# Performance work log

Measured on AMD Instinct MI355X. Metric: run time of the kernel, lower is better.

Reference implementation:

```python
import jax, jax.numpy as jnp
import numpy as np

N, E, D, L = 50000, 800000, 256, 3  # nodes, edges, feature dim, layers


def setup_inputs() -> dict:
    key = jax.random.key(0)
    k = jax.random.split(key, 5)
    edge_index = jax.random.randint(k[0], (2, E), 0, N)  # row0=src, row1=tgt (PyG COO)
    x_init = jax.random.normal(k[1], (N, D), dtype=jnp.float32)
    s = 1.0 / np.sqrt(D).astype(np.float32)  # Glorot-ish init scale
    W_l = jax.random.uniform(k[2], (L, D, D), minval=-s, maxval=s, dtype=jnp.float32)
    W_r = jax.random.uniform(k[3], (L, D, D), minval=-s, maxval=s, dtype=jnp.float32)
    b = jnp.zeros((L, D), dtype=jnp.float32)
    return {"edge_index": edge_index, "x_init": x_init, "W_l": W_l, "W_r": W_r, "b": b}


def reference(edge_index, x_init, W_l, W_r, b):
    src, tgt = edge_index[0], edge_index[1]
    # mean-aggregation normalizer, computed once (degree of each target node)
    deg = jax.ops.segment_sum(jnp.ones((E,), jnp.float32), tgt, num_segments=N)
    inv_deg = jnp.where(deg > 0, 1.0 / deg, 0.0)[:, None]  # [N,1]

    def sage_conv(x, i):
        # PyG SAGEConv (aggr='mean'): out = lin_l(mean_j x_j) + lin_r(x_i)
        agg = jax.ops.segment_sum(x[src], tgt, num_segments=N) * inv_deg  # [N,D]
        return agg @ W_l[i] + x @ W_r[i] + b[i]

    x = x_init
    x_list = []
    for i in range(L - 1):
        x = jax.nn.relu(sage_conv(x, i) + x)  # residual then ReLU
        x_list.append(x)
        # dropout p=0.0 -> identity
    x = sage_conv(x, L - 1) + x  # final layer with residual, no ReLU
    x_list.append(x)
    return jnp.concatenate(x_list, axis=1)  # [N, L*D] concat of all layer outputs
```

## Files before the change

kernel.cpp:

```cpp
#include <hip/hip_runtime.h>
#include <hip/hip_bf16.h>
#include <stdint.h>

#define NN 50000
#define EE 800000
#define DD 256
#define LL 3
#define NBLK 49
#define NPAD 50176

using floatx4 = __attribute__((ext_vector_type(4))) float;
using shortx8 = __attribute__((ext_vector_type(8))) short;

union U8 { shortx8 v; uint32_t u[4]; };

typedef __attribute__((address_space(1))) const unsigned int gu32;
typedef __attribute__((address_space(3))) unsigned int lu32;
__device__ __forceinline__ void async_copy16(const void* g, void* l) {
    __builtin_amdgcn_global_load_lds((gu32*)g, (lu32*)l, 16, 0, 0);
}

__device__ __forceinline__ uint16_t f2bf(float f) {
    __hip_bfloat16 h = __float2bfloat16(f);
    return *reinterpret_cast<uint16_t*>(&h);
}
__device__ __forceinline__ float bf2f(uint32_t u) {
    union { uint32_t u32; float f; } cv; cv.u32 = (u & 0xffffu) << 16; return cv.f;
}

__global__ void k_count(const int* __restrict__ tgt, int* __restrict__ deg) {
    int e = blockIdx.x * 256 + threadIdx.x;
    if (e < EE) atomicAdd(&deg[tgt[e]], 1);
}

__global__ void k_scan1(const int* __restrict__ deg, int* __restrict__ row_start,
                        int* __restrict__ bsum) {
    __shared__ int wsum[16];
    int t = threadIdx.x, w = t >> 6, lane = t & 63;
    int i = blockIdx.x * 1024 + t;
    int v = (i < NN) ? deg[i] : 0;
    int s = v;
#pragma unroll
    for (int off = 1; off < 64; off <<= 1) {
        int u = __shfl_up(s, off);
        if (lane >= off) s += u;
    }
    if (lane == 63) wsum[w] = s;
    __syncthreads();
    if (t < 16) {
        int ws = wsum[t];
#pragma unroll
        for (int off = 1; off < 16; off <<= 1) {
            int u = __shfl_up(ws, off);
            if (t >= off) ws += u;
        }
        wsum[t] = ws;
    }
    __syncthreads();
    int off = (w > 0) ? wsum[w - 1] : 0;
    if (i < NN) row_start[i] = off + s - v;
    if (t == 1023) bsum[blockIdx.x] = off + s;
}

__global__ void k_scan2(int* __restrict__ bsum, int* __restrict__ row_start) {
    int t = threadIdx.x;
    int v = (t < NBLK) ? bsum[t] : 0;
    int s = v;
#pragma unroll
    for (int off = 1; off < 64; off <<= 1) {
        int u = __shfl_up(s, off);
        if (t >= off) s += u;
    }
    if (t < NBLK) bsum[t] = s - v;
    if (t == 0) row_start[NN] = EE;
}

__global__ void k_init2(const int* __restrict__ deg, const int* __restrict__ bsum,
                        int* __restrict__ row_start, int* __restrict__ cursor,
                        float* __restrict__ invd) {
    int i = blockIdx.x * 1024 + threadIdx.x;
    if (i < NN) {
        int r = row_start[i] + bsum[blockIdx.x];
        row_start[i] = r;
        cursor[i] = r;
        int d = deg[i];
        invd[i] = d > 0 ? 1.0f / (float)d : 0.0f;
    }
}

__global__ void k_scatter(const int* __restrict__ src, const int* __restrict__ tgt,
                          int* __restrict__ cursor, int* __restrict__ csr) {
    int e = blockIdx.x * 256 + threadIdx.x;
    if (e < EE) {
        int p = atomicAdd(&cursor[tgt[e]], 1);
        csr[p] = src[e];
    }
}

__global__ void k_wprep(const float* __restrict__ Wl, const float* __restrict__ Wr,
                        uint16_t* __restrict__ wtl_hi, uint16_t* __restrict__ wtl_lo,
                        uint16_t* __restrict__ wtr_hi, uint16_t* __restrict__ wtr_lo) {
    int d = blockIdx.x * 256 + threadIdx.x;
    int i = d >> 16, n = (d >> 8) & 255, k = d & 255;
    int s = (i << 16) | (k << 8) | n;
    float wl = Wl[s];
    float wr = Wr[s] + ((n == k) ? 1.0f : 0.0f);
    uint32_t ul = __float_as_uint(wl), ur = __float_as_uint(wr);
    wtl_hi[d] = (uint16_t)(ul >> 16);
    wtl_lo[d] = f2bf(wl - __uint_as_float(ul & 0xFFFF0000u));
    wtr_hi[d] = (uint16_t)(ur >> 16);
    wtr_lo[d] = f2bf(wr - __uint_as_float(ur & 0xFFFF0000u));
}

__global__ void k_split0(const float* __restrict__ x, uint16_t* __restrict__ xs2) {
    int t = threadIdx.x;
    int row = blockIdx.x * 4 + (t >> 6);
    int col = (t & 63) * 4;
    uint32_t h01 = 0, h23 = 0, l01 = 0, l23 = 0;
    if (row < NN) {
        float4 v = *reinterpret_cast<const float4*>(x + (size_t)row * DD + col);
        uint32_t u0 = __float_as_uint(v.x), u1 = __float_as_uint(v.y);
        uint32_t u2 = __float_as_uint(v.z), u3 = __float_as_uint(v.w);
        h01 = (u0 >> 16) | (u1 & 0xFFFF0000u);
        h23 = (u2 >> 16) | (u3 & 0xFFFF0000u);
        l01 = (uint32_t)f2bf(v.x - __uint_as_float(u0 & 0xFFFF0000u))
            | ((uint32_t)f2bf(v.y - __uint_as_float(u1 & 0xFFFF0000u)) << 16);
        l23 = (uint32_t)f2bf(v.z - __uint_as_float(u2 & 0xFFFF0000u))
            | ((uint32_t)f2bf(v.w - __uint_as_float(u3 & 0xFFFF0000u)) << 16);
    }
    *reinterpret_cast<uint2*>(xs2 + (size_t)row * 512 + col) = make_uint2(h01, h23);
    *reinterpret_cast<uint2*>(xs2 + (size_t)row * 512 + 256 + col) = make_uint2(l01, l23);
}

__global__ __launch_bounds__(256, 2) void k_gemm4(
    const uint16_t* __restrict__ xs2,
    const uint16_t* __restrict__ whl, const uint16_t* __restrict__ whr,
    const uint16_t* __restrict__ wll, const uint16_t* __restrict__ wlr,
    const float* __restrict__ bias,
    uint16_t* __restrict__ yl, float* __restrict__ outz)
{
    extern __shared__ __align__(16) char smem[];
    int bid = blockIdx.x;
    int cg = bid / 200;
    int rg = bid - cg * 200;
    if (rg >= 196) return;
    int t = threadIdx.x;
    int wave = t >> 6, lane = t & 63, quad = lane >> 4, l16 = lane & 15;
    int row0 = rg * 256, col0 = cg * 32;

    {
        const uint16_t* mp0 = whl + col0 * 256;
        const uint16_t* mp1 = whr + col0 * 256;
        const uint16_t* mp2 = wll + col0 * 256;
        const uint16_t* mp3 = wlr + col0 * 256;
        int nrow = t >> 5;
        int soff = ((t & 31) ^ nrow) * 8;
#pragma unroll
        for (int i = 0; i < 4; ++i) {
            int go = (i * 8 + nrow) * 256 + soff;
            char* d = smem + i * 4096 + t * 16;
            async_copy16(mp0 + go, d);
            async_copy16(mp1 + go, d + 16384);
            async_copy16(mp2 + go, d + 32768);
            async_copy16(mp3 + go, d + 49152);
        }
    }

    const uint16_t* ap[4];
#pragma unroll
    for (int rt = 0; rt < 4; ++rt)
        ap[rt] = xs2 + (size_t)(row0 + wave * 64 + rt * 16 + l16) * 512 + quad * 8;

    floatx4 accy[4][2], accz[4][2];
#pragma unroll
    for (int rt = 0; rt < 4; ++rt)
#pragma unroll
        for (int ct = 0; ct < 2; ++ct) {
            accy[rt][ct] = (floatx4){0.f, 0.f, 0.f, 0.f};
            accz[rt][ct] = (floatx4){0.f, 0.f, 0.f, 0.f};
        }

    U8 abuf[3][4];
#pragma unroll
    for (int rt = 0; rt < 4; ++rt) {
        abuf[0][rt].v = *reinterpret_cast<const shortx8*>(ap[rt]);
        abuf[1][rt].v = *reinterpret_cast<const shortx8*>(ap[rt] + 32);
    }

    __syncthreads();

    int bbase0 = l16 * 512;
    int bbase1 = (16 + l16) * 512;
    int bxor = l16 & 7;

#pragma unroll
    for (int c = 0; c < 16; ++c) {
        if (c < 14) {
#pragma unroll
            for (int rt = 0; rt < 4; ++rt)
                abuf[(c + 2) % 3][rt].v =
                    *reinterpret_cast<const shortx8*>(ap[rt] + (c + 2) * 32);
        }
        int kk = c & 7;
        int so = ((kk * 4 + quad) ^ bxor) * 16;
        shortx8 b00 = *reinterpret_cast<const shortx8*>(smem + bbase0 + so);
        shortx8 b10 = *reinterpret_cast<const shortx8*>(smem + bbase1 + so);
        shortx8 b01 = *reinterpret_cast<const shortx8*>(smem + 16384 + bbase0 + so);
        shortx8 b11 = *reinterpret_cast<const shortx8*>(smem + 16384 + bbase1 + so);
        shortx8 c00, c10, c01, c11;
        if (c < 8) {
            c00 = *reinterpret_cast<const shortx8*>(smem + 32768 + bbase0 + so);
            c10 = *reinterpret_cast<const shortx8*>(smem + 32768 + bbase1 + so);
            c01 = *reinterpret_cast<const shortx8*>(smem + 49152 + bbase0 + so);
            c11 = *reinterpret_cast<const shortx8*>(smem + 49152 + bbase1 + so);
        }
#pragma unroll
        for (int rt = 0; rt < 4; ++rt) {
            shortx8 a = abuf[c % 3][rt].v;
            accy[rt][0] = __builtin_amdgcn_mfma_f32_16x16x32_bf16(a, b00, accy[rt][0], 0, 0, 0);
            accy[rt][1] = __builtin_amdgcn_mfma_f32_16x16x32_bf16(a, b10, accy[rt][1], 0, 0, 0);
            accz[rt][0] = __builtin_amdgcn_mfma_f32_16x16x32_bf16(a, b01, accz[rt][0], 0, 0, 0);
            accz[rt][1] = __builtin_amdgcn_mfma_f32_16x16x32_bf16(a, b11, accz[rt][1], 0, 0, 0);
            if (c < 8) {
                accy[rt][0] = __builtin_amdgcn_mfma_f32_16x16x32_bf16(a, c00, accy[rt][0], 0, 0, 0);
                accy[rt][1] = __builtin_amdgcn_mfma_f32_16x16x32_bf16(a, c10, accy[rt][1], 0, 0, 0);
                accz[rt][0] = __builtin_amdgcn_mfma_f32_16x16x32_bf16(a, c01, accz[rt][0], 0, 0, 0);
                accz[rt][1] = __builtin_amdgcn_mfma_f32_16x16x32_bf16(a, c11, accz[rt][1], 0, 0, 0);
            }
        }
    }

    float bct[2] = { bias[col0 + l16], bias[col0 + 16 + l16] };
#pragma unroll
    for (int rt = 0; rt < 4; ++rt) {
#pragma unroll
        for (int ct = 0; ct < 2; ++ct) {
            int colg = col0 + ct * 16 + l16;
#pragma unroll
            for (int r = 0; r < 4; ++r) {
                int rowg = row0 + wave * 64 + rt * 16 + quad * 4 + r;
                if (rowg < NN) {
                    yl[(size_t)rowg * 256 + colg] = f2bf(accy[rt][ct][r]);
                    outz[(size_t)rowg * (LL * DD) + colg] = accz[rt][ct][r] + bct[ct];
                }
            }
        }
    }
}

__global__ __launch_bounds__(256) void k_finish(
    const int* __restrict__ rs, const int* __restrict__ csr,
    const float* __restrict__ invd, const uint16_t* __restrict__ yl,
    uint16_t* __restrict__ xs2, float* __restrict__ outz,
    int do_relu, int wsplit)
{
    int node = blockIdx.x * 4 + (threadIdx.x >> 6);
    int lane = threadIdx.x & 63;
    int col = lane * 4;
    int s = rs[node], e = rs[node + 1];
    float w = invd[node];
    float* zp = outz + (size_t)node * (LL * DD) + col;
    float4 z = *reinterpret_cast<const float4*>(zp);
    float a0 = 0.f, a1 = 0.f, a2 = 0.f, a3 = 0.f;
    int p = s;
    for (; p + 8 <= e; p += 8) {
        int i0 = csr[p],     i1 = csr[p + 1], i2 = csr[p + 2], i3 = csr[p + 3];
        int i4 = csr[p + 4], i5 = csr[p + 5], i6 = csr[p + 6], i7 = csr[p + 7];
        uint2 v0 = *reinterpret_cast<const uint2*>(yl + (size_t)i0 * 256 + col);
        uint2 v1 = *reinterpret_cast<const uint2*>(yl + (size_t)i1 * 256 + col);
        uint2 v2 = *reinterpret_cast<const uint2*>(yl + (size_t)i2 * 256 + col);
        uint2 v3 = *reinterpret_cast<const uint2*>(yl + (size_t)i3 * 256 + col);
        uint2 v4 = *reinterpret_cast<const uint2*>(yl + (size_t)i4 * 256 + col);
        uint2 v5 = *reinterpret_cast<const uint2*>(yl + (size_t)i5 * 256 + col);
        uint2 v6 = *reinterpret_cast<const uint2*>(yl + (size_t)i6 * 256 + col);
        uint2 v7 = *reinterpret_cast<const uint2*>(yl + (size_t)i7 * 256 + col);
        a0 += ((bf2f(v0.x) + bf2f(v1.x)) + (bf2f(v2.x) + bf2f(v3.x)))
            + ((bf2f(v4.x) + bf2f(v5.x)) + (bf2f(v6.x) + bf2f(v7.x)));
        a1 += ((bf2f(v0.x >> 16) + bf2f(v1.x >> 16)) + (bf2f(v2.x >> 16) + bf2f(v3.x >> 16)))
            + ((bf2f(v4.x >> 16) + bf2f(v5.x >> 16)) + (bf2f(v6.x >> 16) + bf2f(v7.x >> 16)));
        a2 += ((bf2f(v0.y) + bf2f(v1.y)) + (bf2f(v2.y) + bf2f(v3.y)))
            + ((bf2f(v4.y) + bf2f(v5.y)) + (bf2f(v6.y) + bf2f(v7.y)));
        a3 += ((bf2f(v0.y >> 16) + bf2f(v1.y >> 16)) + (bf2f(v2.y >> 16) + bf2f(v3.y >> 16)))
            + ((bf2f(v4.y >> 16) + bf2f(v5.y >> 16)) + (bf2f(v6.y >> 16) + bf2f(v7.y >> 16)));
    }
    for (; p + 4 <= e; p += 4) {
        int i0 = csr[p], i1 = csr[p + 1], i2 = csr[p + 2], i3 = csr[p + 3];
        uint2 v0 = *reinterpret_cast<const uint2*>(yl + (size_t)i0 * 256 + col);
        uint2 v1 = *reinterpret_cast<const uint2*>(yl + (size_t)i1 * 256 + col);
        uint2 v2 = *reinterpret_cast<const uint2*>(yl + (size_t)i2 * 256 + col);
        uint2 v3 = *reinterpret_cast<const uint2*>(yl + (size_t)i3 * 256 + col);
        a0 += (bf2f(v0.x) + bf2f(v1.x)) + (bf2f(v2.x) + bf2f(v3.x));
        a1 += (bf2f(v0.x >> 16) + bf2f(v1.x >> 16)) + (bf2f(v2.x >> 16) + bf2f(v3.x >> 16));
        a2 += (bf2f(v0.y) + bf2f(v1.y)) + (bf2f(v2.y) + bf2f(v3.y));
        a3 += (bf2f(v0.y >> 16) + bf2f(v1.y >> 16)) + (bf2f(v2.y >> 16) + bf2f(v3.y >> 16));
    }
    for (; p < e; ++p) {
        int i = csr[p];
        uint2 v = *reinterpret_cast<const uint2*>(yl + (size_t)i * 256 + col);
        a0 += bf2f(v.x); a1 += bf2f(v.x >> 16); a2 += bf2f(v.y); a3 += bf2f(v.y >> 16);
    }
    float o0 = z.x + w * a0;
    float o1 = z.y + w * a1;
    float o2 = z.z + w * a2;
    float o3 = z.w + w * a3;
    if (do_relu) {
        o0 = fmaxf(o0, 0.f); o1 = fmaxf(o1, 0.f);
        o2 = fmaxf(o2, 0.f); o3 = fmaxf(o3, 0.f);
    }
    *reinterpret_cast<float4*>(zp) = make_float4(o0, o1, o2, o3);
    if (wsplit) {
        uint32_t u0 = __float_as_uint(o0), u1 = __float_as_uint(o1);
        uint32_t u2 = __float_as_uint(o2), u3 = __float_as_uint(o3);
        uint32_t h01 = (u0 >> 16) | (u1 & 0xFFFF0000u);
        uint32_t h23 = (u2 >> 16) | (u3 & 0xFFFF0000u);
        uint32_t l01 = (uint32_t)f2bf(o0 - __uint_as_float(u0 & 0xFFFF0000u))
                     | ((uint32_t)f2bf(o1 - __uint_as_float(u1 & 0xFFFF0000u)) << 16);
        uint32_t l23 = (uint32_t)f2bf(o2 - __uint_as_float(u2 & 0xFFFF0000u))
                     | ((uint32_t)f2bf(o3 - __uint_as_float(u3 & 0xFFFF0000u)) << 16);
        *reinterpret_cast<uint2*>(xs2 + (size_t)node * 512 + col) = make_uint2(h01, h23);
        *reinterpret_cast<uint2*>(xs2 + (size_t)node * 512 + 256 + col) = make_uint2(l01, l23);
    }
}

extern "C" void kernel_launch(void* const* d_in, const int* in_sizes, int n_in,
                              void* d_out, int out_size, void* d_ws, size_t ws_size,
                              hipStream_t stream) {
    const int*   edge   = (const int*)d_in[0];
    const float* x_init = (const float*)d_in[1];
    const float* W_l    = (const float*)d_in[2];
    const float* W_r    = (const float*)d_in[3];
    const float* bias   = (const float*)d_in[4];
    float*       out    = (float*)d_out;

    char* ws = (char*)d_ws;
    int*      degI      = (int*)(ws + 0x0000000);
    int*      row_start = (int*)(ws + 0x0040000);
    int*      cursor    = (int*)(ws + 0x0080000);
    float*    invd      = (float*)(ws + 0x00C0000);
    int*      bsum      = (int*)(ws + 0x0100000);
    int*      csr       = (int*)(ws + 0x0140000);
    uint16_t* whl       = (uint16_t*)(ws + 0x0480000);
    uint16_t* whr       = (uint16_t*)(ws + 0x04E0000);
    uint16_t* wll       = (uint16_t*)(ws + 0x0540000);
    uint16_t* wlr       = (uint16_t*)(ws + 0x05A0000);
    uint16_t* yl        = (uint16_t*)(ws + 0x0600000);
    uint16_t* xs2       = (uint16_t*)(ws + 0x1E80000);

    hipMemsetAsync(degI, 0, NN * sizeof(int), stream);
    k_count<<<(EE + 255) / 256, 256, 0, stream>>>(edge + EE, degI);
    k_scan1<<<NBLK, 1024, 0, stream>>>(degI, row_start, bsum);
    k_scan2<<<1, 64, 0, stream>>>(bsum, row_start);
    k_init2<<<NBLK, 1024, 0, stream>>>(degI, bsum, row_start, cursor, invd);
    k_scatter<<<(EE + 255) / 256, 256, 0, stream>>>(edge, edge + EE, cursor, csr);
    k_wprep<<<(LL * DD * DD) / 256, 256, 0, stream>>>(W_l, W_r, whl, wll, whr, wlr);
    k_split0<<<NPAD / 4, 256, 0, stream>>>(x_init, xs2);

    for (int i = 0; i < LL; ++i) {
        size_t wo = (size_t)i * DD * DD;
        k_gemm4<<<1600, 256, 65536, stream>>>(
            xs2, whl + wo, whr + wo, wll + wo, wlr + wo, bias + (size_t)i * DD,
            yl, out + (size_t)i * DD);
        k_finish<<<NN / 4, 256, 0, stream>>>(
            row_start, csr, invd, yl, xs2,
            out + (size_t)i * DD, (i < LL - 1) ? 1 : 0, (i < LL - 1) ? 1 : 0);
    }
}
```

Before: 716.0 us.

## Fuse preprocessing kernels and tile gather by 32-column panels

Merges degree counting, weight splitting and input splitting into one launch to cut launch overhead. Restructures the aggregation kernel so each block handles 32 nodes over one 32-column panel, with 8 threads per node, to improve cache locality of the gathered rows across blocks sharing a panel. The cost is that each node's CSR indices and metadata are re-read 8 times, and gathers become narrower per node.

```diff
diff --git a/kernel.cpp b/kernel.cpp
--- a/kernel.cpp
+++ b/kernel.cpp
@@ -8,6 +8,10 @@
 #define LL 3
 #define NBLK 49
 #define NPAD 50176
+#define PNB 1563
+#define CNT_BLKS ((EE + 255) / 256)
+#define WPREP_BLKS ((LL * DD * DD) / 256)
+#define SPLIT_BLKS (NPAD / 4)
 
 using floatx4 = __attribute__((ext_vector_type(4))) float;
 using shortx8 = __attribute__((ext_vector_type(8))) short;
@@ -26,11 +30,6 @@
 }
 __device__ __forceinline__ float bf2f(uint32_t u) {
     union { uint32_t u32; float f; } cv; cv.u32 = (u & 0xffffu) << 16; return cv.f;
-}
-
-__global__ void k_count(const int* __restrict__ tgt, int* __restrict__ deg) {
-    int e = blockIdx.x * 256 + threadIdx.x;
-    if (e < EE) atomicAdd(&deg[tgt[e]], 1);
 }
 
 __global__ void k_scan1(const int* __restrict__ deg, int* __restrict__ row_start,
@@ -97,39 +96,45 @@
     }
 }
 
-__global__ void k_wprep(const float* __restrict__ Wl, const float* __restrict__ Wr,
-                        uint16_t* __restrict__ wtl_hi, uint16_t* __restrict__ wtl_lo,
-                        uint16_t* __restrict__ wtr_hi, uint16_t* __restrict__ wtr_lo) {
-    int d = blockIdx.x * 256 + threadIdx.x;
-    int i = d >> 16, n = (d >> 8) & 255, k = d & 255;
-    int s = (i << 16) | (k << 8) | n;
-    float wl = Wl[s];
-    float wr = Wr[s] + ((n == k) ? 1.0f : 0.0f);
-    uint32_t ul = __float_as_uint(wl), ur = __float_as_uint(wr);
-    wtl_hi[d] = (uint16_t)(ul >> 16);
-    wtl_lo[d] = f2bf(wl - __uint_as_float(ul & 0xFFFF0000u));
-    wtr_hi[d] = (uint16_t)(ur >> 16);
-    wtr_lo[d] = f2bf(wr - __uint_as_float(ur & 0xFFFF0000u));
-}
-
-__global__ void k_split0(const float* __restrict__ x, uint16_t* __restrict__ xs2) {
-    int t = threadIdx.x;
-    int row = blockIdx.x * 4 + (t >> 6);
-    int col = (t & 63) * 4;
-    uint32_t h01 = 0, h23 = 0, l01 = 0, l23 = 0;
-    if (row < NN) {
-        float4 v = *reinterpret_cast<const float4*>(x + (size_t)row * DD + col);
-        uint32_t u0 = __float_as_uint(v.x), u1 = __float_as_uint(v.y);
-        uint32_t u2 = __float_as_uint(v.z), u3 = __float_as_uint(v.w);
-        h01 = (u0 >> 16) | (u1 & 0xFFFF0000u);
-        h23 = (u2 >> 16) | (u3 & 0xFFFF0000u);
-        l01 = (uint32_t)f2bf(v.x - __uint_as_float(u0 & 0xFFFF0000u))
-            | ((uint32_t)f2bf(v.y - __uint_as_float(u1 & 0xFFFF0000u)) << 16);
-        l23 = (uint32_t)f2bf(v.z - __uint_as_float(u2 & 0xFFFF0000u))
-            | ((uint32_t)f2bf(v.w - __uint_as_float(u3 & 0xFFFF0000u)) << 16);
-    }
-    *reinterpret_cast<uint2*>(xs2 + (size_t)row * 512 + col) = make_uint2(h01, h23);
-    *reinterpret_cast<uint2*>(xs2 + (size_t)row * 512 + 256 + col) = make_uint2(l01, l23);
+__global__ void k_pre(const int* __restrict__ tgt, int* __restrict__ deg,
+                      const float* __restrict__ Wl, const float* __restrict__ Wr,
+                      uint16_t* __restrict__ wtl_hi, uint16_t* __restrict__ wtl_lo,
+                      uint16_t* __restrict__ wtr_hi, uint16_t* __restrict__ wtr_lo,
+                      const float* __restrict__ x, uint16_t* __restrict__ xs2) {
+    int b = blockIdx.x, t = threadIdx.x;
+    if (b < CNT_BLKS) {
+        int e = b * 256 + t;
+        if (e < EE) atomicAdd(&deg[tgt[e]], 1);
+    } else if (b < CNT_BLKS + WPREP_BLKS) {
+        int d = (b - CNT_BLKS) * 256 + t;
+        int i = d >> 16, n = (d >> 8) & 255, k = d & 255;
+        int s = (i << 16) | (k << 8) | n;
+        float wl = Wl[s];
+        float wr = Wr[s] + ((n == k) ? 1.0f : 0.0f);
+        uint32_t ul = __float_as_uint(wl), ur = __float_as_uint(wr);
+        wtl_hi[d] = (uint16_t)(ul >> 16);
+        wtl_lo[d] = f2bf(wl - __uint_as_float(ul & 0xFFFF0000u));
+        wtr_hi[d] = (uint16_t)(ur >> 16);
+        wtr_lo[d] = f2bf(wr - __uint_as_float(ur & 0xFFFF0000u));
+    } else {
+        int bb = b - CNT_BLKS - WPREP_BLKS;
+        int row = bb * 4 + (t >> 6);
+        int col = (t & 63) * 4;
+        uint32_t h01 = 0, h23 = 0, l01 = 0, l23 = 0;
+        if (row < NN) {
+            float4 v = *reinterpret_cast<const float4*>(x + (size_t)row * DD + col);
+            uint32_t u0 = __float_as_uint(v.x), u1 = __float_as_uint(v.y);
+            uint32_t u2 = __float_as_uint(v.z), u3 = __float_as_uint(v.w);
+            h01 = (u0 >> 16) | (u1 & 0xFFFF0000u);
+            h23 = (u2 >> 16) | (u3 & 0xFFFF0000u);
+            l01 = (uint32_t)f2bf(v.x - __uint_as_float(u0 & 0xFFFF0000u))
+                | ((uint32_t)f2bf(v.y - __uint_as_float(u1 & 0xFFFF0000u)) << 16);
+            l23 = (uint32_t)f2bf(v.z - __uint_as_float(u2 & 0xFFFF0000u))
+                | ((uint32_t)f2bf(v.w - __uint_as_float(u3 & 0xFFFF0000u)) << 16);
+        }
+        *reinterpret_cast<uint2*>(xs2 + (size_t)row * 512 + col) = make_uint2(h01, h23);
+        *reinterpret_cast<uint2*>(xs2 + (size_t)row * 512 + 256 + col) = make_uint2(l01, l23);
+    }
 }
 
 __global__ __launch_bounds__(256, 2) void k_gemm4(
@@ -254,26 +259,32 @@
     uint16_t* __restrict__ xs2, float* __restrict__ outz,
     int do_relu, int wsplit)
 {
-    int node = blockIdx.x * 4 + (threadIdx.x >> 6);
-    int lane = threadIdx.x & 63;
-    int col = lane * 4;
+    int bid = blockIdx.x;
+    int panel = bid & 7;
+    int nb = bid >> 3;
+    int t = threadIdx.x;
+    int node = nb * 32 + (t >> 3);
+    if (node >= NN) return;
+    int sub = t & 7;
+    int col = panel * 32 + sub * 4;
     int s = rs[node], e = rs[node + 1];
     float w = invd[node];
     float* zp = outz + (size_t)node * (LL * DD) + col;
     float4 z = *reinterpret_cast<const float4*>(zp);
+    const uint16_t* ylc = yl + col;
     float a0 = 0.f, a1 = 0.f, a2 = 0.f, a3 = 0.f;
     int p = s;
     for (; p + 8 <= e; p += 8) {
         int i0 = csr[p],     i1 = csr[p + 1], i2 = csr[p + 2], i3 = csr[p + 3];
         int i4 = csr[p + 4], i5 = csr[p + 5], i6 = csr[p + 6], i7 = csr[p + 7];
-        uint2 v0 = *reinterpret_cast<const uint2*>(yl + (size_t)i0 * 256 + col);
-        uint2 v1 = *reinterpret_cast<const uint2*>(yl + (size_t)i1 * 256 + col);
-        uint2 v2 = *reinterpret_cast<const uint2*>(yl + (size_t)i2 * 256 + col);
-        uint2 v3 = *reinterpret_cast<const uint2*>(yl + (size_t)i3 * 256 + col);
-        uint2 v4 = *reinterpret_cast<const uint2*>(yl + (size_t)i4 * 256 + col);
-        uint2 v5 = *reinterpret_cast<const uint2*>(yl + (size_t)i5 * 256 + col);
-        uint2 v6 = *reinterpret_cast<const uint2*>(yl + (size_t)i6 * 256 + col);
-        uint2 v7 = *reinterpret_cast<const uint2*>(yl + (size_t)i7 * 256 + col);
+        uint2 v0 = *reinterpret_cast<const uint2*>(ylc + (size_t)i0 * 256);
+        uint2 v1 = *reinterpret_cast<const uint2*>(ylc + (size_t)i1 * 256);
+        uint2 v2 = *reinterpret_cast<const uint2*>(ylc + (size_t)i2 * 256);
+        uint2 v3 = *reinterpret_cast<const uint2*>(ylc + (size_t)i3 * 256);
+        uint2 v4 = *reinterpret_cast<const uint2*>(ylc + (size_t)i4 * 256);
+        uint2 v5 = *reinterpret_cast<const uint2*>(ylc + (size_t)i5 * 256);
+        uint2 v6 = *reinterpret_cast<const uint2*>(ylc + (size_t)i6 * 256);
+        uint2 v7 = *reinterpret_cast<const uint2*>(ylc + (size_t)i7 * 256);
         a0 += ((bf2f(v0.x) + bf2f(v1.x)) + (bf2f(v2.x) + bf2f(v3.x)))
             + ((bf2f(v4.x) + bf2f(v5.x)) + (bf2f(v6.x) + bf2f(v7.x)));
         a1 += ((bf2f(v0.x >> 16) + bf2f(v1.x >> 16)) + (bf2f(v2.x >> 16) + bf2f(v3.x >> 16)))
@@ -285,10 +296,10 @@
     }
     for (; p + 4 <= e; p += 4) {
         int i0 = csr[p], i1 = csr[p + 1], i2 = csr[p + 2], i3 = csr[p + 3];
-        uint2 v0 = *reinterpret_cast<const uint2*>(yl + (size_t)i0 * 256 + col);
-        uint2 v1 = *reinterpret_cast<const uint2*>(yl + (size_t)i1 * 256 + col);
-        uint2 v2 = *reinterpret_cast<const uint2*>(yl + (size_t)i2 * 256 + col);
-        uint2 v3 = *reinterpret_cast<const uint2*>(yl + (size_t)i3 * 256 + col);
+        uint2 v0 = *reinterpret_cast<const uint2*>(ylc + (size_t)i0 * 256);
+        uint2 v1 = *reinterpret_cast<const uint2*>(ylc + (size_t)i1 * 256);
+        uint2 v2 = *reinterpret_cast<const uint2*>(ylc + (size_t)i2 * 256);
+        uint2 v3 = *reinterpret_cast<const uint2*>(ylc + (size_t)i3 * 256);
         a0 += (bf2f(v0.x) + bf2f(v1.x)) + (bf2f(v2.x) + bf2f(v3.x));
         a1 += (bf2f(v0.x >> 16) + bf2f(v1.x >> 16)) + (bf2f(v2.x >> 16) + bf2f(v3.x >> 16));
         a2 += (bf2f(v0.y) + bf2f(v1.y)) + (bf2f(v2.y) + bf2f(v3.y));
@@ -296,7 +307,7 @@
     }
     for (; p < e; ++p) {
         int i = csr[p];
-        uint2 v = *reinterpret_cast<const uint2*>(yl + (size_t)i * 256 + col);
+        uint2 v = *reinterpret_cast<const uint2*>(ylc + (size_t)i * 256);
         a0 += bf2f(v.x); a1 += bf2f(v.x >> 16); a2 += bf2f(v.y); a3 += bf2f(v.y >> 16);
     }
     float o0 = z.x + w * a0;
@@ -347,20 +358,19 @@
     uint16_t* xs2       = (uint16_t*)(ws + 0x1E80000);
 
     hipMemsetAsync(degI, 0, NN * sizeof(int), stream);
-    k_count<<<(EE + 255) / 256, 256, 0, stream>>>(edge + EE, degI);
+    k_pre<<<CNT_BLKS + WPREP_BLKS + SPLIT_BLKS, 256, 0, stream>>>(
+        edge + EE, degI, W_l, W_r, whl, wll, whr, wlr, x_init, xs2);
     k_scan1<<<NBLK, 1024, 0, stream>>>(degI, row_start, bsum);
     k_scan2<<<1, 64, 0, stream>>>(bsum, row_start);
     k_init2<<<NBLK, 1024, 0, stream>>>(degI, bsum, row_start, cursor, invd);
     k_scatter<<<(EE + 255) / 256, 256, 0, stream>>>(edge, edge + EE, cursor, csr);
-    k_wprep<<<(LL * DD * DD) / 256, 256, 0, stream>>>(W_l, W_r, whl, wll, whr, wlr);
-    k_split0<<<NPAD / 4, 256, 0, stream>>>(x_init, xs2);
 
     for (int i = 0; i < LL; ++i) {
         size_t wo = (size_t)i * DD * DD;
         k_gemm4<<<1600, 256, 65536, stream>>>(
             xs2, whl + wo, whr + wo, wll + wo, wlr + wo, bias + (size_t)i * DD,
             yl, out + (size_t)i * DD);
-        k_finish<<<NN / 4, 256, 0, stream>>>(
+        k_finish<<<8 * PNB, 256, 0, stream>>>(
             row_start, csr, invd, yl, xs2,
             out + (size_t)i * DD, (i < LL - 1) ? 1 : 0, (i < LL - 1) ? 1 : 0);
     }
```

New measurement: 771.8 us. +7.8%, slower.

## Merge preprocessing kernels, single-block scan, deepen A-operand prefetch in GEMM

Applied to the files above, without the earlier changes.

Folds degree counting, weight splitting and input splitting into one multi-role kernel. It also replaces the three-kernel scan (block scan, block-sum scan, fixup) with a single 1024-thread block that loops over tiles with a carry. Together these cut the launch count from 7 preprocessing kernels to 3. Separately, the GEMM A-operand register prefetch ring grows from 3 to 5 stages so global loads are issued further ahead. This raises register pressure, and the serial single-block scan may be slower than the parallel version.

```diff
diff --git a/kernel.cpp b/kernel.cpp
--- a/kernel.cpp
+++ b/kernel.cpp
@@ -8,6 +8,9 @@
 #define LL 3
 #define NBLK 49
 #define NPAD 50176
+#define CNT_BLKS ((EE + 255) / 256)
+#define WPREP_BLKS ((LL * DD * DD) / 256)
+#define SPLIT_BLKS (NPAD / 4)
 
 using floatx4 = __attribute__((ext_vector_type(4))) float;
 using shortx8 = __attribute__((ext_vector_type(8))) short;
@@ -28,64 +31,90 @@
     union { uint32_t u32; float f; } cv; cv.u32 = (u & 0xffffu) << 16; return cv.f;
 }
 
-__global__ void k_count(const int* __restrict__ tgt, int* __restrict__ deg) {
-    int e = blockIdx.x * 256 + threadIdx.x;
-    if (e < EE) atomicAdd(&deg[tgt[e]], 1);
-}
-
-__global__ void k_scan1(const int* __restrict__ deg, int* __restrict__ row_start,
-                        int* __restrict__ bsum) {
+__global__ void k_pre(const int* __restrict__ tgt, int* __restrict__ deg,
+                      const float* __restrict__ Wl, const float* __restrict__ Wr,
+                      uint16_t* __restrict__ wtl_hi, uint16_t* __restrict__ wtl_lo,
+                      uint16_t* __restrict__ wtr_hi, uint16_t* __restrict__ wtr_lo,
+                      const float* __restrict__ x, uint16_t* __restrict__ xs2) {
+    int b = blockIdx.x, t = threadIdx.x;
+    if (b < CNT_BLKS) {
+        int e = b * 256 + t;
+        if (e < EE) atomicAdd(&deg[tgt[e]], 1);
+    } else if (b < CNT_BLKS + WPREP_BLKS) {
+        int d = (b - CNT_BLKS) * 256 + t;
+        int i = d >> 16, n = (d >> 8) & 255, k = d & 255;
+        int s = (i << 16) | (k << 8) | n;
+        float wl = Wl[s];
+        float wr = Wr[s] + ((n == k) ? 1.0f : 0.0f);
+        uint32_t ul = __float_as_uint(wl), ur = __float_as_uint(wr);
+        wtl_hi[d] = (uint16_t)(ul >> 16);
+        wtl_lo[d] = f2bf(wl - __uint_as_float(ul & 0xFFFF0000u));
+        wtr_hi[d] = (uint16_t)(ur >> 16);
+        wtr_lo[d] = f2bf(wr - __uint_as_float(ur & 0xFFFF0000u));
+    } else {
+        int bb = b - CNT_BLKS - WPREP_BLKS;
+        int row = bb * 4 + (t >> 6);
+        int col = (t & 63) * 4;
+        uint32_t h01 = 0, h23 = 0, l01 = 0, l23 = 0;
+        if (row < NN) {
+            float4 v = *reinterpret_cast<const float4*>(x + (size_t)row * DD + col);
+            uint32_t u0 = __float_as_uint(v.x), u1 = __float_as_uint(v.y);
+            uint32_t u2 = __float_as_uint(v.z), u3 = __float_as_uint(v.w);
+            h01 = (u0 >> 16) | (u1 & 0xFFFF0000u);
+            h23 = (u2 >> 16) | (u3 & 0xFFFF0000u);
+            l01 = (uint32_t)f2bf(v.x - __uint_as_float(u0 & 0xFFFF0000u))
+                | ((uint32_t)f2bf(v.y - __uint_as_float(u1 & 0xFFFF0000u)) << 16);
+            l23 = (uint32_t)f2bf(v.z - __uint_as_float(u2 & 0xFFFF0000u))
+                | ((uint32_t)f2bf(v.w - __uint_as_float(u3 & 0xFFFF0000u)) << 16);
+        }
+        *reinterpret_cast<uint2*>(xs2 + (size_t)row * 512 + col) = make_uint2(h01, h23);
+        *reinterpret_cast<uint2*>(xs2 + (size_t)row * 512 + 256 + col) = make_uint2(l01, l23);
+    }
+}
+
+__global__ __launch_bounds__(1024) void k_scanall(const int* __restrict__ deg,
+                                                  int* __restrict__ row_start,
+                                                  int* __restrict__ cursor,
+                                                  float* __restrict__ invd) {
     __shared__ int wsum[16];
+    __shared__ int carry_s;
     int t = threadIdx.x, w = t >> 6, lane = t & 63;
-    int i = blockIdx.x * 1024 + t;
-    int v = (i < NN) ? deg[i] : 0;
-    int s = v;
-#pragma unroll
-    for (int off = 1; off < 64; off <<= 1) {
-        int u = __shfl_up(s, off);
-        if (lane >= off) s += u;
-    }
-    if (lane == 63) wsum[w] = s;
+    if (t == 0) carry_s = 0;
     __syncthreads();
-    if (t < 16) {
-        int ws = wsum[t];
-#pragma unroll
-        for (int off = 1; off < 16; off <<= 1) {
-            int u = __shfl_up(ws, off);
-            if (t >= off) ws += u;
-        }
-        wsum[t] = ws;
-    }
-    __syncthreads();
-    int off = (w > 0) ? wsum[w - 1] : 0;
-    if (i < NN) row_start[i] = off + s - v;
-    if (t == 1023) bsum[blockIdx.x] = off + s;
-}
-
-__global__ void k_scan2(int* __restrict__ bsum, int* __restrict__ row_start) {
-    int t = threadIdx.x;
-    int v = (t < NBLK) ? bsum[t] : 0;
-    int s = v;
-#pragma unroll
-    for (int off = 1; off < 64; off <<= 1) {
-        int u = __shfl_up(s, off);
-        if (t >= off) s += u;
-    }
-    if (t < NBLK) bsum[t] = s - v;
+    for (int tile = 0; tile < NBLK; ++tile) {
+        int i = tile * 1024 + t;
+        int v = (i < NN) ? deg[i] : 0;
+        int s = v;
+#pragma unroll
+        for (int off = 1; off < 64; off <<= 1) {
+            int u = __shfl_up(s, off);
+            if (lane >= off) s += u;
+        }
+        if (lane == 63) wsum[w] = s;
+        __syncthreads();
+        if (t < 16) {
+            int ws = wsum[t];
+#pragma unroll
+            for (int off = 1; off < 16; off <<= 1) {
+                int u = __shfl_up(ws, off);
+                if (t >= off) ws += u;
+            }
+            wsum[t] = ws;
+        }
+        __syncthreads();
+        int off0 = (w > 0) ? wsum[w - 1] : 0;
+        int carry = carry_s;
+        if (i < NN) {
+            int r = carry + off0 + s - v;
+            row_start[i] = r;
+            cursor[i] = r;
+            invd[i] = v > 0 ? 1.0f / (float)v : 0.0f;
+        }
+        __syncthreads();
+        if (t == 1023) carry_s = carry + off0 + s;
+        __syncthreads();
+    }
     if (t == 0) row_start[NN] = EE;
-}
-
-__global__ void k_init2(const int* __restrict__ deg, const int* __restrict__ bsum,
-                        int* __restrict__ row_start, int* __restrict__ cursor,
-                        float* __restrict__ invd) {
-    int i = blockIdx.x * 1024 + threadIdx.x;
-    if (i < NN) {
-        int r = row_start[i] + bsum[blockIdx.x];
-        row_start[i] = r;
-        cursor[i] = r;
-        int d = deg[i];
-        invd[i] = d > 0 ? 1.0f / (float)d : 0.0f;
-    }
 }
 
 __global__ void k_scatter(const int* __restrict__ src, const int* __restrict__ tgt,
@@ -95,41 +124,6 @@
         int p = atomicAdd(&cursor[tgt[e]], 1);
         csr[p] = src[e];
     }
-}
-
-__global__ void k_wprep(const float* __restrict__ Wl, const float* __restrict__ Wr,
-                        uint16_t* __restrict__ wtl_hi, uint16_t* __restrict__ wtl_lo,
-                        uint16_t* __restrict__ wtr_hi, uint16_t* __restrict__ wtr_lo) {
-    int d = blockIdx.x * 256 + threadIdx.x;
-    int i = d >> 16, n = (d >> 8) & 255, k = d & 255;
-    int s = (i << 16) | (k << 8) | n;
-    float wl = Wl[s];
-    float wr = Wr[s] + ((n == k) ? 1.0f : 0.0f);
-    uint32_t ul = __float_as_uint(wl), ur = __float_as_uint(wr);
-    wtl_hi[d] = (uint16_t)(ul >> 16);
-    wtl_lo[d] = f2bf(wl - __uint_as_float(ul & 0xFFFF0000u));
-    wtr_hi[d] = (uint16_t)(ur >> 16);
-    wtr_lo[d] = f2bf(wr - __uint_as_float(ur & 0xFFFF0000u));
-}
-
-__global__ void k_split0(const float* __restrict__ x, uint16_t* __restrict__ xs2) {
-    int t = threadIdx.x;
-    int row = blockIdx.x * 4 + (t >> 6);
-    int col = (t & 63) * 4;
-    uint32_t h01 = 0, h23 = 0, l01 = 0, l23 = 0;
-    if (row < NN) {
-        float4 v = *reinterpret_cast<const float4*>(x + (size_t)row * DD + col);
-        uint32_t u0 = __float_as_uint(v.x), u1 = __float_as_uint(v.y);
-        uint32_t u2 = __float_as_uint(v.z), u3 = __float_as_uint(v.w);
-        h01 = (u0 >> 16) | (u1 & 0xFFFF0000u);
-        h23 = (u2 >> 16) | (u3 & 0xFFFF0000u);
-        l01 = (uint32_t)f2bf(v.x - __uint_as_float(u0 & 0xFFFF0000u))
-            | ((uint32_t)f2bf(v.y - __uint_as_float(u1 & 0xFFFF0000u)) << 16);
-        l23 = (uint32_t)f2bf(v.z - __uint_as_float(u2 & 0xFFFF0000u))
-            | ((uint32_t)f2bf(v.w - __uint_as_float(u3 & 0xFFFF0000u)) << 16);
-    }
-    *reinterpret_cast<uint2*>(xs2 + (size_t)row * 512 + col) = make_uint2(h01, h23);
-    *reinterpret_cast<uint2*>(xs2 + (size_t)row * 512 + 256 + col) = make_uint2(l01, l23);
 }
 
 __global__ __launch_bounds__(256, 2) void k_gemm4(
@@ -180,11 +174,13 @@
             accz[rt][ct] = (floatx4){0.f, 0.f, 0.f, 0.f};
         }
 
-    U8 abuf[3][4];
+    U8 abuf[5][4];
 #pragma unroll
     for (int rt = 0; rt < 4; ++rt) {
         abuf[0][rt].v = *reinterpret_cast<const shortx8*>(ap[rt]);
         abuf[1][rt].v = *reinterpret_cast<const shortx8*>(ap[rt] + 32);
+        abuf[2][rt].v = *reinterpret_cast<const shortx8*>(ap[rt] + 64);
+        abuf[3][rt].v = *reinterpret_cast<const shortx8*>(ap[rt] + 96);
     }
 
     __syncthreads();
@@ -195,11 +191,11 @@
 
 #pragma unroll
     for (int c = 0; c < 16; ++c) {
-        if (c < 14) {
+        if (c < 12) {
 #pragma unroll
             for (int rt = 0; rt < 4; ++rt)
-                abuf[(c + 2) % 3][rt].v =
-                    *reinterpret_cast<const shortx8*>(ap[rt] + (c + 2) * 32);
+                abuf[(c + 4) % 5][rt].v =
+                    *reinterpret_cast<const shortx8*>(ap[rt] + (c + 4) * 32);
         }
         int kk = c & 7;
         int so = ((kk * 4 + quad) ^ bxor) * 16;
@@ -216,7 +212,7 @@
         }
 #pragma unroll
         for (int rt = 0; rt < 4; ++rt) {
-            shortx8 a = abuf[c % 3][rt].v;
+            shortx8 a = abuf[c % 5][rt].v;
             accy[rt][0] = __builtin_amdgcn_mfma_f32_16x16x32_bf16(a, b00, accy[rt][0], 0, 0, 0);
             accy[rt][1] = __builtin_amdgcn_mfma_f32_16x16x32_bf16(a, b10, accy[rt][1], 0, 0, 0);
             accz[rt][0] = __builtin_amdgcn_mfma_f32_16x16x32_bf16(a, b01, accz[rt][0], 0, 0, 0);
@@ -337,7 +333,6 @@
     int*      row_start = (int*)(ws + 0x0040000);
     int*      cursor    = (int*)(ws + 0x0080000);
     float*    invd      = (float*)(ws + 0x00C0000);
-    int*      bsum      = (int*)(ws + 0x0100000);
     int*      csr       = (int*)(ws + 0x0140000);
     uint16_t* whl       = (uint16_t*)(ws + 0x0480000);
     uint16_t* whr       = (uint16_t*)(ws + 0x04E0000);
@@ -347,13 +342,10 @@
     uint16_t* xs2       = (uint16_t*)(ws + 0x1E80000);
 
     hipMemsetAsync(degI, 0, NN * sizeof(int), stream);
-    k_count<<<(EE + 255) / 256, 256, 0, stream>>>(edge + EE, degI);
-    k_scan1<<<NBLK, 1024, 0, stream>>>(degI, row_start, bsum);
-    k_scan2<<<1, 64, 0, stream>>>(bsum, row_start);
-    k_init2<<<NBLK, 1024, 0, stream>>>(degI, bsum, row_start, cursor, invd);
+    k_pre<<<CNT_BLKS + WPREP_BLKS + SPLIT_BLKS, 256, 0, stream>>>(
+        edge + EE, degI, W_l, W_r, whl, wll, whr, wlr, x_init, xs2);
+    k_scanall<<<1, 1024, 0, stream>>>(degI, row_start, cursor, invd);
     k_scatter<<<(EE + 255) / 256, 256, 0, stream>>>(edge, edge + EE, cursor, csr);
-    k_wprep<<<(LL * DD * DD) / 256, 256, 0, stream>>>(W_l, W_r, whl, wll, whr, wlr);
-    k_split0<<<NPAD / 4, 256, 0, stream>>>(x_init, xs2);
 
     for (int i = 0; i < LL; ++i) {
         size_t wo = (size_t)i * DD * DD;
```

Result: slower. 748.8 us (+4.6%).
